# Optimization experiments

Hardware: AMD Instinct MI355X
Metric: run time of the kernel (lower is better)

## Reference

```python
import jax, jax.numpy as jnp
import numpy as np

B, S = 16, 1                 # decode phase: one new token per sequence
NUM_HEADS, HEAD_DIM = 16, 64
HIDDEN = NUM_HEADS * HEAD_DIM
BLOCK_SIZE = 16
MAX_CTX = 4096               # padded context length (max over sequences)
BLOCKS_PER_SEQ = MAX_CTX // BLOCK_SIZE
MAX_BLOCKS = B * BLOCKS_PER_SEQ


def setup_inputs() -> dict:
    key = jax.random.key(0)
    ks = jax.random.split(key, 8)
    hidden_states = jax.random.normal(ks[0], (B, S, HIDDEN), jnp.float32)
    key_cache = jax.random.normal(ks[1], (MAX_BLOCKS, BLOCK_SIZE, NUM_HEADS, HEAD_DIM), jnp.float32)
    value_cache = jax.random.normal(ks[2], (MAX_BLOCKS, BLOCK_SIZE, NUM_HEADS, HEAD_DIM), jnp.float32)
    # each sequence owns a disjoint set of physical blocks (order = allocation order)
    block_table = jnp.arange(B * BLOCKS_PER_SEQ, dtype=jnp.int32).reshape(B, BLOCKS_PER_SEQ)
    positions = jax.random.randint(ks[3], (B,), 0, MAX_CTX, dtype=jnp.int32)
    wscale = 1.0 / np.sqrt(HIDDEN).astype(np.float32)
    Wq = jax.random.normal(ks[4], (HIDDEN, HIDDEN), jnp.float32) * wscale
    Wk = jax.random.normal(ks[5], (HIDDEN, HIDDEN), jnp.float32) * wscale
    Wv = jax.random.normal(ks[6], (HIDDEN, HIDDEN), jnp.float32) * wscale
    Wo = jax.random.normal(ks[7], (HIDDEN, HIDDEN), jnp.float32) * wscale
    return {
        "hidden_states": hidden_states,
        "key_cache": key_cache,
        "value_cache": value_cache,
        "block_table": block_table,
        "positions": positions,
        "Wq": Wq, "Wk": Wk, "Wv": Wv, "Wo": Wo,
    }


def reference(hidden_states, key_cache, value_cache, block_table, positions, Wq, Wk, Wv, Wo):
    scale = HEAD_DIM ** -0.5
    # projections (torch nn.Linear: x @ W.T)
    q = (hidden_states @ Wq.T).reshape(B, S, NUM_HEADS, HEAD_DIM)
    k_new = (hidden_states @ Wk.T).reshape(B, S, NUM_HEADS, HEAD_DIM)
    v_new = (hidden_states @ Wv.T).reshape(B, S, NUM_HEADS, HEAD_DIM)

    # store_kv: scatter the new token's K/V into the paged cache
    bidx = jnp.arange(B)
    blk = block_table[bidx, positions // BLOCK_SIZE]   # [B]
    slot = positions % BLOCK_SIZE                       # [B]
    key_cache = key_cache.at[blk, slot].set(k_new[:, 0])
    value_cache = value_cache.at[blk, slot].set(v_new[:, 0])

    # get_kv: gather the full (padded) context through the block table
    tok = jnp.arange(MAX_CTX)
    gb = block_table[:, tok // BLOCK_SIZE]              # [B, T] physical block per token
    gs = (tok % BLOCK_SIZE)[None, :]                    # [1, T] slot within block
    K = key_cache[gb, gs]                               # [B, T, H, D]
    V = value_cache[gb, gs]                             # [B, T, H, D]

    # attention with causal/length mask: token t visible iff t <= pos
    scores = jnp.einsum('bqhd,bkhd->bhqk', q, K) * scale   # [B, H, 1, T]
    mask = tok[None, :] <= positions[:, None]               # [B, T]
    scores = jnp.where(mask[:, None, None, :], scores, -jnp.inf)
    attn = jax.nn.softmax(scores, axis=-1)
    out = jnp.einsum('bhqk,bkhd->bqhd', attn, V).reshape(B, S, HIDDEN)
    return out @ Wo.T
```

## Files before the change

kernel.cpp:

```cpp
#include <hip/hip_runtime.h>
#include <math.h>

#define BATCH 16
#define NUM_HEADS 16
#define HEAD_DIM 64
#define HIDDEN 1024
#define BLOCK_SIZE 16
#define MAX_CTX 4096
#define BLOCKS_PER_SEQ 256
#define SPLITS 16
#define CHUNKS 4
#define CHUNK_F4 64

#define AO_OFF   0
#define PML_OFF  16384
#define PO_OFF   24576
#define PART_OFF 286720

#define LOG2E 1.4426950408889634f

__global__ void proj_partial(const float* __restrict__ X,
                             const float* __restrict__ W0,
                             const float* __restrict__ W1,
                             const float* __restrict__ W2,
                             float* __restrict__ part) {
    const int tid = threadIdx.x;
    const int b = tid & 15;
    const int r = tid >> 4;
    const int row = blockIdx.x * 16 + r;
    const int c = blockIdx.y;
    const int m = row >> 10;
    const int row_in = row & 1023;
    const float* W = (m == 0) ? W0 : (m == 1) ? W1 : W2;

    const float4* wrow = (const float4*)(W + (size_t)row_in * HIDDEN) + c * CHUNK_F4;
    const float4* xrow = (const float4*)(X + (size_t)b * HIDDEN) + c * CHUNK_F4;
    float acc = 0.f;
#pragma unroll 16
    for (int i = 0; i < CHUNK_F4; ++i) {
        float4 w4 = wrow[i];
        float4 x4 = xrow[i];
        acc += w4.x * x4.x + w4.y * x4.y + w4.z * x4.z + w4.w * x4.w;
    }
    part[((size_t)row * 16 + b) * CHUNKS + c] = acc;
}

__global__ void proj_combine(const float* __restrict__ part,
                             float* __restrict__ out) {
    const int idx = blockIdx.x * 256 + threadIdx.x;
    const int row = idx >> 4;
    const int b = idx & 15;
    const float4 p = ((const float4*)part)[idx];
    out[(size_t)b * HIDDEN + row] = p.x + p.y + p.z + p.w;
}

#define LOAD_KV(IT, K0, K1, K2, K3, V0, V1, V2, V3)                              \
    do {                                                                          \
        const int blk_ = bt_lds[(IT) * 4 + w];                                    \
        const size_t base_ = ((size_t)blk_ * BLOCK_SIZE + g) * 1024 + hoff;       \
        const float* kp_ = key_cache + base_;                                     \
        const float* vp_ = value_cache + base_;                                   \
        K0 = *(const float4*)(kp_);                                               \
        K1 = *(const float4*)(kp_ + 4096);                                        \
        K2 = *(const float4*)(kp_ + 8192);                                        \
        K3 = *(const float4*)(kp_ + 12288);                                       \
        V0 = *(const float4*)(vp_);                                               \
        V1 = *(const float4*)(vp_ + 4096);                                        \
        V2 = *(const float4*)(vp_ + 8192);                                        \
        V3 = *(const float4*)(vp_ + 12288);                                       \
    } while (0)

#define COMPUTE(IT, K0, K1, K2, K3, V0, V1, V2, V3)                               \
    do {                                                                          \
        float d0_ = K0.x * q4.x + K0.y * q4.y + K0.z * q4.z + K0.w * q4.w;        \
        float d1_ = K1.x * q4.x + K1.y * q4.y + K1.z * q4.z + K1.w * q4.w;        \
        float d2_ = K2.x * q4.x + K2.y * q4.y + K2.z * q4.z + K2.w * q4.w;        \
        float d3_ = K3.x * q4.x + K3.y * q4.y + K3.z * q4.z + K3.w * q4.w;        \
        d0_ += __shfl_xor(d0_, 1); d1_ += __shfl_xor(d1_, 1);                     \
        d2_ += __shfl_xor(d2_, 1); d3_ += __shfl_xor(d3_, 1);                     \
        d0_ += __shfl_xor(d0_, 2); d1_ += __shfl_xor(d1_, 2);                     \
        d2_ += __shfl_xor(d2_, 2); d3_ += __shfl_xor(d3_, 2);                     \
        d0_ += __shfl_xor(d0_, 4); d1_ += __shfl_xor(d1_, 4);                     \
        d2_ += __shfl_xor(d2_, 4); d3_ += __shfl_xor(d3_, 4);                     \
        d0_ += __shfl_xor(d0_, 8); d1_ += __shfl_xor(d1_, 8);                     \
        d2_ += __shfl_xor(d2_, 8); d3_ += __shfl_xor(d3_, 8);                     \
        const int tb_ = t0 + (IT) * 64 + w * 16 + g;                              \
        if (tb_ + 0  >= t1) d0_ = -INFINITY;                                      \
        if (tb_ + 4  >= t1) d1_ = -INFINITY;                                      \
        if (tb_ + 8  >= t1) d2_ = -INFINITY;                                      \
        if (tb_ + 12 >= t1) d3_ = -INFINITY;                                      \
        const float mx_ = fmaxf(fmaxf(d0_, d1_), fmaxf(d2_, d3_));                \
        const float m_new_ = fmaxf(m, mx_);                                       \
        const float corr_ = exp2f(m - m_new_);                                    \
        const float p0_ = exp2f(d0_ - m_new_);                                    \
        const float p1_ = exp2f(d1_ - m_new_);                                    \
        const float p2_ = exp2f(d2_ - m_new_);                                    \
        const float p3_ = exp2f(d3_ - m_new_);                                    \
        l = l * corr_ + ((p0_ + p1_) + (p2_ + p3_));                              \
        o4.x = o4.x * corr_ + p0_ * V0.x + p1_ * V1.x + p2_ * V2.x + p3_ * V3.x;  \
        o4.y = o4.y * corr_ + p0_ * V0.y + p1_ * V1.y + p2_ * V2.y + p3_ * V3.y;  \
        o4.z = o4.z * corr_ + p0_ * V0.z + p1_ * V1.z + p2_ * V2.z + p3_ * V3.z;  \
        o4.w = o4.w * corr_ + p0_ * V0.w + p1_ * V1.w + p2_ * V2.w + p3_ * V3.w;  \
        m = m_new_;                                                               \
    } while (0)

__global__ void attn_partial(const float* __restrict__ part,
                             const float* __restrict__ key_cache,
                             const float* __restrict__ value_cache,
                             const int* __restrict__ block_table,
                             const int* __restrict__ positions,
                             float* __restrict__ part_ml,
                             float* __restrict__ part_o) {
    const int s = blockIdx.x;
    const int h = blockIdx.y;
    const int b = blockIdx.z;
    const int tid = threadIdx.x;
    const int lane = tid & 63;
    const int w = tid >> 6;
    const int g = lane >> 4;
    const int sub = lane & 15;
    const int gid = w * 4 + g;

    __shared__ int bt_lds[16];
    __shared__ float gm[16];
    __shared__ float gl[16];
    __shared__ float go[16][64];

    const int pos = positions[b];
    const int chunk = ((pos + SPLITS * 64 - 1) / (SPLITS * 64)) * 64;
    const int t0 = s * chunk;
    const int t1 = min(t0 + chunk, pos);
    const int nvalid = t1 - t0;
    const int niter = (nvalid + 63) >> 6;

    const int hbase = h * HEAD_DIM + sub * 4;
    const float4 pq0 = ((const float4*)part)[(hbase + 0) * 16 + b];
    const float4 pq1 = ((const float4*)part)[(hbase + 1) * 16 + b];
    const float4 pq2 = ((const float4*)part)[(hbase + 2) * 16 + b];
    const float4 pq3 = ((const float4*)part)[(hbase + 3) * 16 + b];

    if (tid < 16) {
        bt_lds[tid] = block_table[b * BLOCKS_PER_SEQ + (t0 >> 4) + tid];
    }
    __syncthreads();

    const float qs = 0.125f * LOG2E;
    float4 q4;
    q4.x = (pq0.x + pq0.y + pq0.z + pq0.w) * qs;
    q4.y = (pq1.x + pq1.y + pq1.z + pq1.w) * qs;
    q4.z = (pq2.x + pq2.y + pq2.z + pq2.w) * qs;
    q4.w = (pq3.x + pq3.y + pq3.z + pq3.w) * qs;
    const int hoff = h * HEAD_DIM + sub * 4;

    float m = -1e30f;
    float l = 0.f;
    float4 o4 = {0.f, 0.f, 0.f, 0.f};

    float4 kA0, kA1, kA2, kA3, vA0, vA1, vA2, vA3;
    float4 kB0, kB1, kB2, kB3, vB0, vB1, vB2, vB3;

    if (niter > 0) {
        LOAD_KV(0, kA0, kA1, kA2, kA3, vA0, vA1, vA2, vA3);
        int it = 0;
        while (true) {
            if (it + 1 < niter) LOAD_KV(it + 1, kB0, kB1, kB2, kB3, vB0, vB1, vB2, vB3);
            COMPUTE(it, kA0, kA1, kA2, kA3, vA0, vA1, vA2, vA3);
            ++it;
            if (it >= niter) break;
            if (it + 1 < niter) LOAD_KV(it + 1, kA0, kA1, kA2, kA3, vA0, vA1, vA2, vA3);
            COMPUTE(it, kB0, kB1, kB2, kB3, vB0, vB1, vB2, vB3);
            ++it;
            if (it >= niter) break;
        }
    }

    go[gid][sub * 4 + 0] = o4.x;
    go[gid][sub * 4 + 1] = o4.y;
    go[gid][sub * 4 + 2] = o4.z;
    go[gid][sub * 4 + 3] = o4.w;
    if (sub == 0) { gm[gid] = m; gl[gid] = l; }
    __syncthreads();

    if (tid < 64) {
        const int d = tid;
        float M = -1e30f;
#pragma unroll
        for (int gi = 0; gi < 16; ++gi) M = fmaxf(M, gm[gi]);
        float L = 0.f, O = 0.f;
#pragma unroll
        for (int gi = 0; gi < 16; ++gi) {
            const float sc = exp2f(gm[gi] - M);
            L += gl[gi] * sc;
            O += go[gi][d] * sc;
        }
        const int pidx = (b * NUM_HEADS + h) * SPLITS + s;
        part_o[(size_t)pidx * 64 + d] = O;
        if (d == 0) {
            part_ml[pidx * 2 + 0] = M;
            part_ml[pidx * 2 + 1] = L;
        }
    }
}

__global__ void attn_reduce(const float* __restrict__ part,
                            const float* __restrict__ part_ml,
                            const float* __restrict__ part_o,
                            float* __restrict__ attn_out) {
    const int bh = blockIdx.x;
    const int b = bh >> 4;
    const int h = bh & 15;
    const int d = threadIdx.x;

    const int row = h * HEAD_DIM + d;
    const float4 pq = ((const float4*)part)[(0    + row) * 16 + b];
    const float4 pk = ((const float4*)part)[(1024 + row) * 16 + b];
    const float4 pv = ((const float4*)part)[(2048 + row) * 16 + b];
    const float qd = pq.x + pq.y + pq.z + pq.w;
    const float kd = pk.x + pk.y + pk.z + pk.w;
    const float vd = pv.x + pv.y + pv.z + pv.w;

    float pr = qd * kd;
    pr += __shfl_xor(pr, 1);
    pr += __shfl_xor(pr, 2);
    pr += __shfl_xor(pr, 4);
    pr += __shfl_xor(pr, 8);
    pr += __shfl_xor(pr, 16);
    pr += __shfl_xor(pr, 32);
    const float s_new = pr * (0.125f * LOG2E);

    float M = s_new;
#pragma unroll
    for (int sp = 0; sp < SPLITS; ++sp)
        M = fmaxf(M, part_ml[(bh * SPLITS + sp) * 2]);

    float L = exp2f(s_new - M);
    float O = L * vd;
#pragma unroll
    for (int sp = 0; sp < SPLITS; ++sp) {
        const float mg = part_ml[(bh * SPLITS + sp) * 2 + 0];
        const float lg = part_ml[(bh * SPLITS + sp) * 2 + 1];
        const float sc = exp2f(mg - M);
        L += lg * sc;
        O += part_o[(size_t)(bh * SPLITS + sp) * 64 + d] * sc;
    }
    attn_out[(size_t)b * HIDDEN + h * HEAD_DIM + d] = O / L;
}

extern "C" void kernel_launch(void* const* d_in, const int* in_sizes, int n_in,
                              void* d_out, int out_size, void* d_ws, size_t ws_size,
                              hipStream_t stream) {
    const float* hidden      = (const float*)d_in[0];
    const float* key_cache   = (const float*)d_in[1];
    const float* value_cache = (const float*)d_in[2];
    const int*   block_table = (const int*)d_in[3];
    const int*   positions   = (const int*)d_in[4];
    const float* Wq          = (const float*)d_in[5];
    const float* Wk          = (const float*)d_in[6];
    const float* Wv          = (const float*)d_in[7];
    const float* Wo          = (const float*)d_in[8];
    float* out = (float*)d_out;

    float* ws = (float*)d_ws;
    float* ao_ws = ws + AO_OFF;
    float* pml   = ws + PML_OFF;
    float* po    = ws + PO_OFF;
    float* part  = ws + PART_OFF;

    proj_partial<<<dim3(192, CHUNKS), 256, 0, stream>>>(hidden, Wq, Wk, Wv, part);

    attn_partial<<<dim3(SPLITS, NUM_HEADS, BATCH), 256, 0, stream>>>(
        part, key_cache, value_cache, block_table, positions, pml, po);

    attn_reduce<<<BATCH * NUM_HEADS, 64, 0, stream>>>(part, pml, po, ao_ws);

    proj_partial<<<dim3(64, CHUNKS), 256, 0, stream>>>(ao_ws, Wo, Wo, Wo, part);
    proj_combine<<<64, 256, 0, stream>>>(part, out);
}
```

Baseline: 96.03 us.

## Halve attention splits and fuse Wo projection with its reduction

Cuts the split-K attention partitions from 16 to 8, so each split covers twice as many tokens (block-table preload grows to 32 entries), and unrolls the reduce kernel to vector-load the 8 partial (m,l) pairs. It also replaces the two-kernel Wo projection (partial sums plus combine) with one kernel that reduces across 16 lanes by wave shuffle, dropping a launch and a workspace round trip. Fewer splits lower parallelism in the attention kernel for short sequences but shrink the reduce work. The new Wo kernel reads each Wo row once per batch element, so Wo is re-read 16 times, mostly from cache.

```diff
diff --git a/kernel.cpp b/kernel.cpp
--- a/kernel.cpp
+++ b/kernel.cpp
@@ -8,14 +8,14 @@
 #define BLOCK_SIZE 16
 #define MAX_CTX 4096
 #define BLOCKS_PER_SEQ 256
-#define SPLITS 16
+#define SPLITS 8
 #define CHUNKS 4
 #define CHUNK_F4 64
 
-#define AO_OFF   0
-#define PML_OFF  16384
-#define PO_OFF   24576
-#define PART_OFF 286720
+#define PART_OFF 0
+#define PML_OFF  196608
+#define PO_OFF   200704
+#define AO_OFF   331776
 
 #define LOG2E 1.4426950408889634f
 
@@ -43,15 +43,6 @@
         acc += w4.x * x4.x + w4.y * x4.y + w4.z * x4.z + w4.w * x4.w;
     }
     part[((size_t)row * 16 + b) * CHUNKS + c] = acc;
-}
-
-__global__ void proj_combine(const float* __restrict__ part,
-                             float* __restrict__ out) {
-    const int idx = blockIdx.x * 256 + threadIdx.x;
-    const int row = idx >> 4;
-    const int b = idx & 15;
-    const float4 p = ((const float4*)part)[idx];
-    out[(size_t)b * HIDDEN + row] = p.x + p.y + p.z + p.w;
 }
 
 #define LOAD_KV(IT, K0, K1, K2, K3, V0, V1, V2, V3)                              \
@@ -121,7 +112,7 @@
     const int sub = lane & 15;
     const int gid = w * 4 + g;
 
-    __shared__ int bt_lds[16];
+    __shared__ int bt_lds[32];
     __shared__ float gm[16];
     __shared__ float gl[16];
     __shared__ float go[16][64];
@@ -139,7 +130,7 @@
     const float4 pq2 = ((const float4*)part)[(hbase + 2) * 16 + b];
     const float4 pq3 = ((const float4*)part)[(hbase + 3) * 16 + b];
 
-    if (tid < 16) {
+    if (tid < 32) {
         bt_lds[tid] = block_table[b * BLOCKS_PER_SEQ + (t0 >> 4) + tid];
     }
     __syncthreads();
@@ -228,22 +219,59 @@
     pr += __shfl_xor(pr, 32);
     const float s_new = pr * (0.125f * LOG2E);
 
+    float2 ml0 = ((const float2*)part_ml)[bh * SPLITS + 0];
+    float2 ml1 = ((const float2*)part_ml)[bh * SPLITS + 1];
+    float2 ml2 = ((const float2*)part_ml)[bh * SPLITS + 2];
+    float2 ml3 = ((const float2*)part_ml)[bh * SPLITS + 3];
+    float2 ml4 = ((const float2*)part_ml)[bh * SPLITS + 4];
+    float2 ml5 = ((const float2*)part_ml)[bh * SPLITS + 5];
+    float2 ml6 = ((const float2*)part_ml)[bh * SPLITS + 6];
+    float2 ml7 = ((const float2*)part_ml)[bh * SPLITS + 7];
+
     float M = s_new;
+    M = fmaxf(M, fmaxf(fmaxf(ml0.x, ml1.x), fmaxf(ml2.x, ml3.x)));
+    M = fmaxf(M, fmaxf(fmaxf(ml4.x, ml5.x), fmaxf(ml6.x, ml7.x)));
+
+    const float sc0 = exp2f(ml0.x - M), sc1 = exp2f(ml1.x - M);
+    const float sc2 = exp2f(ml2.x - M), sc3 = exp2f(ml3.x - M);
+    const float sc4 = exp2f(ml4.x - M), sc5 = exp2f(ml5.x - M);
+    const float sc6 = exp2f(ml6.x - M), sc7 = exp2f(ml7.x - M);
+
+    const float e_new = exp2f(s_new - M);
+    float L = e_new
+            + ml0.y * sc0 + ml1.y * sc1 + ml2.y * sc2 + ml3.y * sc3
+            + ml4.y * sc4 + ml5.y * sc5 + ml6.y * sc6 + ml7.y * sc7;
+    float O = e_new * vd;
+    const float* po = part_o + (size_t)bh * SPLITS * 64 + d;
+    O += po[0 * 64] * sc0 + po[1 * 64] * sc1 + po[2 * 64] * sc2 + po[3 * 64] * sc3
+       + po[4 * 64] * sc4 + po[5 * 64] * sc5 + po[6 * 64] * sc6 + po[7 * 64] * sc7;
+
+    attn_out[(size_t)b * HIDDEN + h * HEAD_DIM + d] = O / L;
+}
+
+__global__ void wo_proj(const float* __restrict__ ao,
+                        const float* __restrict__ Wo,
+                        float* __restrict__ out) {
+    const int rg = blockIdx.x;
+    const int b = blockIdx.y;
+    const int r = threadIdx.x >> 4;
+    const int c = threadIdx.x & 15;
+    const int row = rg * 16 + r;
+
+    const float4* wrow = (const float4*)(Wo + (size_t)row * HIDDEN) + c * 16;
+    const float4* arow = (const float4*)(ao + (size_t)b * HIDDEN) + c * 16;
+    float acc = 0.f;
 #pragma unroll
-    for (int sp = 0; sp < SPLITS; ++sp)
-        M = fmaxf(M, part_ml[(bh * SPLITS + sp) * 2]);
-
-    float L = exp2f(s_new - M);
-    float O = L * vd;
-#pragma unroll
-    for (int sp = 0; sp < SPLITS; ++sp) {
-        const float mg = part_ml[(bh * SPLITS + sp) * 2 + 0];
-        const float lg = part_ml[(bh * SPLITS + sp) * 2 + 1];
-        const float sc = exp2f(mg - M);
-        L += lg * sc;
-        O += part_o[(size_t)(bh * SPLITS + sp) * 64 + d] * sc;
-    }
-    attn_out[(size_t)b * HIDDEN + h * HEAD_DIM + d] = O / L;
+    for (int i = 0; i < 16; ++i) {
+        float4 w4 = wrow[i];
+        float4 a4 = arow[i];
+        acc += w4.x * a4.x + w4.y * a4.y + w4.z * a4.z + w4.w * a4.w;
+    }
+    acc += __shfl_xor(acc, 1);
+    acc += __shfl_xor(acc, 2);
+    acc += __shfl_xor(acc, 4);
+    acc += __shfl_xor(acc, 8);
+    if (c == 0) out[(size_t)b * HIDDEN + row] = acc;
 }
 
 extern "C" void kernel_launch(void* const* d_in, const int* in_sizes, int n_in,
@@ -261,10 +289,10 @@
     float* out = (float*)d_out;
 
     float* ws = (float*)d_ws;
-    float* ao_ws = ws + AO_OFF;
+    float* part  = ws + PART_OFF;
     float* pml   = ws + PML_OFF;
     float* po    = ws + PO_OFF;
-    float* part  = ws + PART_OFF;
+    float* ao_ws = ws + AO_OFF;
 
     proj_partial<<<dim3(192, CHUNKS), 256, 0, stream>>>(hidden, Wq, Wk, Wv, part);
 
@@ -273,6 +301,5 @@
 
     attn_reduce<<<BATCH * NUM_HEADS, 64, 0, stream>>>(part, pml, po, ao_ws);
 
-    proj_partial<<<dim3(64, CHUNKS), 256, 0, stream>>>(ao_ws, Wo, Wo, Wo, part);
-    proj_combine<<<64, 256, 0, stream>>>(part, out);
-}
+    wo_proj<<<dim3(64, BATCH), 256, 0, stream>>>(ao_ws, Wo, out);
+}
```

Measured after the change: 97.78 us. Within noise of the previous version (+1.8%).
